# Optimization experiments

Hardware: AMD Instinct MI355X
Metric: run time of the kernel (lower is better)

Reference implementation:

```python
import jax, jax.numpy as jnp
import numpy as np

N_NODES = 50000


def gcn_conv(x, src, dst, W, b, n_nodes):
    # PyG GCNConv: add self-loops, symmetric normalization D^-1/2 (A+I) D^-1/2 (x W) + b
    E = src.shape[0]
    deg = jax.ops.segment_sum(jnp.ones((E,), x.dtype), dst, num_segments=n_nodes) + 1.0
    dinv = jax.lax.rsqrt(deg)
    h = x @ W  # [N, H]
    norm = dinv[src] * dinv[dst]  # [E]
    agg = jax.ops.segment_sum(h[src] * norm[:, None], dst, num_segments=n_nodes)
    agg = agg + h * (dinv * dinv)[:, None]  # self-loop contribution
    return agg + b


def setup_inputs() -> dict:
    key = jax.random.key(0)
    ks = jax.random.split(key, 16)
    N, E, D, H, T, O = N_NODES, 800000, 128, 128, 2, 1
    x = jax.random.normal(ks[0], (N, D), jnp.float32)
    edge_index = jax.random.randint(ks[1], (2, E), 0, N, jnp.int32)
    edge_attrs = jax.random.uniform(ks[2], (T, E, 7), jnp.float32)
    s = lambda k, sh: jax.random.normal(k, sh, jnp.float32) * (1.0 / np.sqrt(sh[0]))
    return {
        "x": x, "edge_index": edge_index, "edge_attrs": edge_attrs,
        "W1": s(ks[3], (D, H)), "b1": jnp.zeros((H,), jnp.float32),
        "W2": s(ks[4], (H, H)), "b2": jnp.zeros((H,), jnp.float32),
        "W3": s(ks[5], (H, H)), "b3": jnp.zeros((H,), jnp.float32),
        "We": s(ks[6], (2 * H + 7, H)), "be": jnp.zeros((H,), jnp.float32),
        "Wg": s(ks[7], (H, O)), "bg": jnp.zeros((O,), jnp.float32),
    }


def reference(x, edge_index, edge_attrs, W1, b1, W2, b2, W3, b3, We, be, Wg, bg):
    src, dst = edge_index[0], edge_index[1]
    n = x.shape[0]
    outputs = []
    for t in range(edge_attrs.shape[0]):  # small fixed T, x evolves across iterations
        edge_attr = edge_attrs[t]
        x = jax.nn.relu(gcn_conv(x, src, dst, W1, b1, n))
        x = jax.nn.relu(gcn_conv(x, src, dst, W2, b2, n))
        x = jax.nn.relu(gcn_conv(x, src, dst, W3, b3, n))
        # gather-concat-MLP-mean per edge
        edge_features = jnp.concatenate([x[src], x[dst], edge_attr], axis=1)
        edge_output = jax.nn.relu(edge_features @ We + be)
        graph_features = jnp.mean(edge_output, axis=0, keepdims=True)  # [1, H]
        outputs.append(graph_features @ Wg + bg)
        W1 = W2  # no-op placeholder removed below
        W1 = W1  # keep W1 unchanged
    return jnp.concatenate(outputs, axis=0)  # [T, output_dim]
```

## Files before the change

kernel.cpp:

```cpp
#include <hip/hip_runtime.h>
#include <hip/hip_bf16.h>


typedef __attribute__((ext_vector_type(8))) short bf16x8;
typedef __attribute__((ext_vector_type(4))) float f32x4;
typedef __attribute__((ext_vector_type(2))) float f32x2;

__device__ __forceinline__ unsigned short f2bf(float f) {
    union { float f; unsigned int u; } v; v.f = f;
    unsigned int r = v.u + 0x7fffu + ((v.u >> 16) & 1u);
    return (unsigned short)(r >> 16);
}
__device__ __forceinline__ unsigned int pk2bf(float lo, float hi) {
    return (unsigned int)f2bf(lo) | ((unsigned int)f2bf(hi) << 16);
}
__device__ __forceinline__ unsigned char f2fp8(float f) {
    return (unsigned char)(__builtin_amdgcn_cvt_pk_fp8_f32(f, f, 0, false) & 0xff);
}
__device__ __forceinline__ void fp8x4(unsigned int u, float* o) {
    f32x2 lo = __builtin_amdgcn_cvt_pk_f32_fp8(u, false);
    f32x2 hi = __builtin_amdgcn_cvt_pk_f32_fp8(u, true);
    o[0] = lo[0]; o[1] = lo[1]; o[2] = hi[0]; o[3] = hi[1];
}
__device__ __forceinline__ void de16add(uint4 v, float* a) {
    float t[4];
    fp8x4(v.x, t); a[0]+=t[0]; a[1]+=t[1]; a[2]+=t[2]; a[3]+=t[3];
    fp8x4(v.y, t); a[4]+=t[0]; a[5]+=t[1]; a[6]+=t[2]; a[7]+=t[3];
    fp8x4(v.z, t); a[8]+=t[0]; a[9]+=t[1]; a[10]+=t[2]; a[11]+=t[3];
    fp8x4(v.w, t); a[12]+=t[0]; a[13]+=t[1]; a[14]+=t[2]; a[15]+=t[3];
}

__global__ void to_bf16(const float* __restrict__ in, unsigned short* __restrict__ out, int n4)
{
    int i = blockIdx.x * 256 + threadIdx.x;
    if (i < n4) {
        float4 v = ((const float4*)in)[i];
        ushort4 o;
        o.x = f2bf(v.x); o.y = f2bf(v.y); o.z = f2bf(v.z); o.w = f2bf(v.w);
        ((ushort4*)out)[i] = o;
    }
}

__global__ void transpose_w(
    const float* __restrict__ W1, const float* __restrict__ W2,
    const float* __restrict__ W3, const float* __restrict__ We,
    unsigned short* __restrict__ T1, unsigned short* __restrict__ T2,
    unsigned short* __restrict__ T3, unsigned short* __restrict__ Tuv)
{
    const float* src; unsigned short* dst;
    switch (blockIdx.y) {
        case 0:  src = W1;             dst = T1;               break;
        case 1:  src = W2;             dst = T2;               break;
        case 2:  src = W3;             dst = T3;               break;
        case 3:  src = We;             dst = Tuv;              break;
        case 4:  src = We + 128 * 128; dst = Tuv + 128 * 128;  break;
        default: src = W2;             dst = Tuv + 256 * 128;  break;
    }
    for (int i = blockIdx.x * 256 + threadIdx.x; i < 128 * 128; i += 256 * gridDim.x) {
        int k = i >> 7, c = i & 127;
        dst[c * 128 + k] = f2bf(src[i]);
    }
}

__global__ __launch_bounds__(256) void mfma_matmul(
    const unsigned short* __restrict__ X, const unsigned short* __restrict__ Wt,
    unsigned char* __restrict__ out, const float* __restrict__ scale, int n_rows)
{
    const int wave = threadIdx.x >> 6;
    const int lane = threadIdx.x & 63;
    const int m = lane & 15;
    const int q = lane >> 4;
    const int r = blockIdx.x * 64 + wave * 16 + m;
    const bool rv = r < n_rows;

    f32x4 acc[8];
    #pragma unroll
    for (int i = 0; i < 8; ++i) acc[i] = (f32x4){0.f, 0.f, 0.f, 0.f};

    #pragma unroll
    for (int k0 = 0; k0 < 128; k0 += 32) {
        bf16x8 a = {};
        if (rv) a = *(const bf16x8*)(X + (size_t)r * 128 + k0 + q * 8);
        #pragma unroll
        for (int ct = 0; ct < 8; ++ct) {
            bf16x8 b = *(const bf16x8*)(Wt + (ct * 16 + m) * 128 + k0 + q * 8);
            acc[ct] = __builtin_amdgcn_mfma_f32_16x16x32_bf16(a, b, acc[ct], 0, 0, 0);
        }
    }

    #pragma unroll
    for (int reg = 0; reg < 4; ++reg) {
        int gr = blockIdx.x * 64 + wave * 16 + q * 4 + reg;
        if (gr >= n_rows) continue;
        float s = scale[gr];
        #pragma unroll
        for (int ct = 0; ct < 8; ++ct)
            out[(size_t)gr * 128 + ct * 16 + m] = f2fp8(acc[ct][reg] * s);
    }
}

#define FPAD 136
#define GN 32
#define ICAP 64
#define ISTR 72
__global__ __launch_bounds__(256) void fused_gm(
    const unsigned char* __restrict__ hs_in, const int* __restrict__ csr_src,
    const int* __restrict__ offs, const int* __restrict__ counts,
    const float* __restrict__ dinv, const float* __restrict__ bias,
    const unsigned short* __restrict__ Wt, int ncols, int uvcols,
    unsigned char* __restrict__ buv, unsigned char* __restrict__ bh, int n)
{
    __shared__ unsigned short xs[GN * FPAD];
    __shared__ int idxl[GN * ISTR];
    const int tid = threadIdx.x;
    const int row = tid >> 3;
    const int node = blockIdx.x * GN + row;
    const int lg = tid & 7;
    const int c16 = lg * 16;

    if (node < n) {
        const int off = offs[node];
        const int cnt = counts[node];
        const int cap = min(cnt, ICAP);

        for (int j = lg; j < cap; j += 8)
            idxl[row * ISTR + j] = csr_src[off + j];

        float a[16] = {};
        de16add(*(const uint4*)(hs_in + (size_t)node * 128 + c16), a);

        int j = 0;
        if (cap >= 4) {
            uint4 hA[4], hB[4];
            #pragma unroll
            for (int q = 0; q < 4; ++q)
                hA[q] = *(const uint4*)(hs_in + (size_t)idxl[row * ISTR + q] * 128 + c16);
            j = 4;
            for (; j + 4 <= cap; j += 4) {
                #pragma unroll
                for (int q = 0; q < 4; ++q)
                    hB[q] = *(const uint4*)(hs_in + (size_t)idxl[row * ISTR + j + q] * 128 + c16);
                #pragma unroll
                for (int q = 0; q < 4; ++q) de16add(hA[q], a);
                #pragma unroll
                for (int q = 0; q < 4; ++q) hA[q] = hB[q];
            }
            #pragma unroll
            for (int q = 0; q < 4; ++q) de16add(hA[q], a);
        }
        for (; j < cap; ++j)
            de16add(*(const uint4*)(hs_in + (size_t)idxl[row * ISTR + j] * 128 + c16), a);
        for (; j < cnt; ++j)
            de16add(*(const uint4*)(hs_in + (size_t)csr_src[off + j] * 128 + c16), a);

        float dn = dinv[node];
        #pragma unroll
        for (int i = 0; i < 4; ++i) {
            float4 bb = *(const float4*)(bias + c16 + i * 4);
            float r0 = fmaxf(fmaf(a[i*4+0], dn, bb.x), 0.f);
            float r1 = fmaxf(fmaf(a[i*4+1], dn, bb.y), 0.f);
            float r2 = fmaxf(fmaf(a[i*4+2], dn, bb.z), 0.f);
            float r3 = fmaxf(fmaf(a[i*4+3], dn, bb.w), 0.f);
            *(unsigned int*)&xs[row * FPAD + c16 + i*4 + 0] = pk2bf(r0, r1);
            *(unsigned int*)&xs[row * FPAD + c16 + i*4 + 2] = pk2bf(r2, r3);
        }
    }
    __syncthreads();

    const int wave = tid >> 6;
    const int lane = tid & 63;
    const int m = lane & 15;
    const int q = lane >> 4;
    const int rt = (wave & 1) * 16;
    const int nct = ncols >> 4;
    const int half = nct >> 1;
    const int ct0 = (wave >> 1) * half;

    for (int ci = 0; ci < half; ++ci) {
        const int ct = ct0 + ci;
        f32x4 acc = (f32x4){0.f, 0.f, 0.f, 0.f};
        #pragma unroll
        for (int k0 = 0; k0 < 128; k0 += 32) {
            bf16x8 a = *(const bf16x8*)&xs[(rt + m) * FPAD + k0 + q * 8];
            bf16x8 b = *(const bf16x8*)(Wt + (size_t)(ct * 16 + m) * 128 + k0 + q * 8);
            acc = __builtin_amdgcn_mfma_f32_16x16x32_bf16(a, b, acc, 0, 0, 0);
        }
        const int col = ct * 16 + m;
        #pragma unroll
        for (int reg = 0; reg < 4; ++reg) {
            int nd = blockIdx.x * GN + rt + q * 4 + reg;
            if (nd >= n) continue;
            if (col < uvcols)
                buv[(size_t)nd * 256 + col] = f2fp8(acc[reg]);
            else
                bh[(size_t)nd * 128 + col - uvcols] = f2fp8(acc[reg] * dinv[nd]);
        }
    }
}

#define EM_CHUNK 256
__global__ __launch_bounds__(256) void edge_mlp(
    const unsigned char* __restrict__ uv, const int* __restrict__ src,
    const int* __restrict__ dst, const float* __restrict__ ea,
    const float* __restrict__ We_e, const float* __restrict__ be,
    const float* __restrict__ Wg, float* __restrict__ acc, int E)
{
    const int tid  = threadIdx.x;
    const int lane = tid & 31;
    const int g    = tid >> 5;
    const int c4   = lane * 4;

    __shared__ float eas[EM_CHUNK * 7];
    __shared__ int   ss[EM_CHUNK];
    __shared__ int   ds[EM_CHUNK];
    __shared__ float red[256];

    float4 w[7];
    #pragma unroll
    for (int i = 0; i < 7; ++i)
        w[i] = *(const float4*)(We_e + i * 128 + c4);
    const float4 be4 = *(const float4*)(be + c4);
    const float4 wg4 = *(const float4*)(Wg + c4);

    float4 part = make_float4(0.f, 0.f, 0.f, 0.f);

    for (int base = blockIdx.x * EM_CHUNK; base < E; base += gridDim.x * EM_CHUNK) {
        const int nch = min(EM_CHUNK, E - base);
        for (int i = tid; i < nch * 7; i += 256)
            eas[i] = ea[(size_t)base * 7 + i];
        for (int i = tid; i < nch; i += 256) {
            ss[i] = src[base + i];
            ds[i] = dst[base + i];
        }
        __syncthreads();

        auto ev = [&](int j) {
            unsigned int us = *(const unsigned int*)(uv + (size_t)ss[j] * 256 + c4);
            unsigned int vs = *(const unsigned int*)(uv + (size_t)ds[j] * 256 + 128 + c4);
            float uf[4], vf[4];
            fp8x4(us, uf); fp8x4(vs, vf);
            const float* eav = &eas[j * 7];
            float4 val;
            val.x = uf[0] + vf[0] + be4.x;
            val.y = uf[1] + vf[1] + be4.y;
            val.z = uf[2] + vf[2] + be4.z;
            val.w = uf[3] + vf[3] + be4.w;
            #pragma unroll
            for (int i = 0; i < 7; ++i) {
                float e = eav[i];
                val.x = fmaf(e, w[i].x, val.x);
                val.y = fmaf(e, w[i].y, val.y);
                val.z = fmaf(e, w[i].z, val.z);
                val.w = fmaf(e, w[i].w, val.w);
            }
            part.x += fmaxf(val.x, 0.f);
            part.y += fmaxf(val.y, 0.f);
            part.z += fmaxf(val.z, 0.f);
            part.w += fmaxf(val.w, 0.f);
        };

        int j = g;
        for (; j + 32 <= nch; j += 32) {
            ev(j); ev(j + 8); ev(j + 16); ev(j + 24);
        }
        for (; j < nch; j += 8)
            ev(j);
        __syncthreads();
    }

    float p = part.x * wg4.x + part.y * wg4.y + part.z * wg4.z + part.w * wg4.w;
    red[tid] = p;
    __syncthreads();
    for (int s = 128; s > 0; s >>= 1) {
        if (tid < s) red[tid] += red[tid + s];
        __syncthreads();
    }
    if (tid == 0) atomicAdd(acc, red[0]);
}

__global__ void count_edges(const int* __restrict__ dst, int* __restrict__ counts, int E)
{
    int e = blockIdx.x * 256 + threadIdx.x;
    if (e < E) atomicAdd(&counts[dst[e]], 1);
}

__global__ void compute_dinv(const int* __restrict__ counts, float* __restrict__ dinv, int n)
{
    int i = blockIdx.x * 256 + threadIdx.x;
    if (i < n) dinv[i] = rsqrtf((float)counts[i] + 1.0f);
}

__global__ void scan1(const int* __restrict__ counts, int* __restrict__ scanned,
                      int* __restrict__ btot, int n)
{
    __shared__ int sh[256];
    int i = blockIdx.x * 256 + threadIdx.x;
    int v = (i < n) ? counts[i] : 0;
    sh[threadIdx.x] = v;
    __syncthreads();
    for (int off = 1; off < 256; off <<= 1) {
        int t = (threadIdx.x >= off) ? sh[threadIdx.x - off] : 0;
        __syncthreads();
        sh[threadIdx.x] += t;
        __syncthreads();
    }
    if (i < n) scanned[i] = sh[threadIdx.x] - v;
    if (threadIdx.x == 255) btot[blockIdx.x] = sh[255];
}

__global__ void scan2(int* __restrict__ btot, int nb)
{
    __shared__ int sh[256];
    int v = (threadIdx.x < nb) ? btot[threadIdx.x] : 0;
    sh[threadIdx.x] = v;
    __syncthreads();
    for (int off = 1; off < 256; off <<= 1) {
        int t = (threadIdx.x >= off) ? sh[threadIdx.x - off] : 0;
        __syncthreads();
        sh[threadIdx.x] += t;
        __syncthreads();
    }
    if (threadIdx.x < nb) btot[threadIdx.x] = sh[threadIdx.x] - v;
}

__global__ void scan3(const int* __restrict__ scanned, const int* __restrict__ btot,
                      int* __restrict__ offs, int* __restrict__ cursor, int n)
{
    int i = blockIdx.x * 256 + threadIdx.x;
    if (i < n) {
        int o = scanned[i] + btot[blockIdx.x];
        offs[i] = o;
        cursor[i] = o;
    }
}

__global__ void fill_csr(const int* __restrict__ src, const int* __restrict__ dst,
                         int* __restrict__ cursor, int* __restrict__ csr_src, int E)
{
    int e = blockIdx.x * 256 + threadIdx.x;
    if (e < E) {
        int slot = atomicAdd(&cursor[dst[e]], 1);
        csr_src[slot] = src[e];
    }
}

__global__ void write_out(const float* __restrict__ acc, const float* __restrict__ bg,
                          float* __restrict__ out, float invE, int T)
{
    int t = threadIdx.x;
    if (t < T) out[t] = acc[t] * invE + bg[0];
}


extern "C" void kernel_launch(void* const* d_in, const int* in_sizes, int n_in,
                              void* d_out, int out_size, void* d_ws, size_t ws_size,
                              hipStream_t stream)
{
    const float* x   = (const float*)d_in[0];
    const int*  eidx = (const int*)d_in[1];
    const float* ea  = (const float*)d_in[2];
    const float* W1  = (const float*)d_in[3];
    const float* b1  = (const float*)d_in[4];
    const float* W2  = (const float*)d_in[5];
    const float* b2  = (const float*)d_in[6];
    const float* W3  = (const float*)d_in[7];
    const float* b3  = (const float*)d_in[8];
    const float* We  = (const float*)d_in[9];
    const float* be  = (const float*)d_in[10];
    const float* Wg  = (const float*)d_in[11];
    const float* bg  = (const float*)d_in[12];

    const int N = in_sizes[0] / 128;
    const int E = in_sizes[1] / 2;
    const int T = in_sizes[2] / (E * 7);
    const int* src = eidx;
    const int* dst = eidx + E;

    char* wsp = (char*)d_ws;
    auto alloc = [&](size_t bytes) -> char* {
        char* p = wsp;
        wsp += (bytes + 255) / 256 * 256;
        return p;
    };
    int*   counts  = (int*)alloc((size_t)N * 4);
    int*   offs    = (int*)alloc((size_t)N * 4);
    int*   cursor  = (int*)alloc((size_t)N * 4);
    int*   scanned = (int*)alloc((size_t)N * 4);
    int*   btot    = (int*)alloc(1024);
    int*   csr_src = (int*)alloc((size_t)E * 4);
    float* dinv    = (float*)alloc((size_t)N * 4);
    float* acc     = (float*)alloc(256);
    unsigned short* X0  = (unsigned short*)alloc((size_t)N * 128 * 2);
    unsigned char*  Bh0 = (unsigned char*)alloc((size_t)N * 128);
    unsigned char*  Bh1 = (unsigned char*)alloc((size_t)N * 128);
    unsigned char*  Buv = (unsigned char*)alloc((size_t)N * 256);
    unsigned short* T1  = (unsigned short*)alloc(128 * 128 * 2);
    unsigned short* T2  = (unsigned short*)alloc(128 * 128 * 2);
    unsigned short* T3  = (unsigned short*)alloc(128 * 128 * 2);
    unsigned short* Tuv = (unsigned short*)alloc(384 * 128 * 2);

    hipMemsetAsync(counts, 0, (size_t)N * 4, stream);
    hipMemsetAsync(acc, 0, (size_t)T * 4, stream);

    to_bf16<<<(N * 128 / 4 + 255) / 256, 256, 0, stream>>>(x, X0, N * 128 / 4);
    transpose_w<<<dim3(8, 6), 256, 0, stream>>>(W1, W2, W3, We, T1, T2, T3, Tuv);

    count_edges<<<(E + 255) / 256, 256, 0, stream>>>(dst, counts, E);
    compute_dinv<<<(N + 255) / 256, 256, 0, stream>>>(counts, dinv, N);
    const int nb = (N + 255) / 256;
    scan1<<<nb, 256, 0, stream>>>(counts, scanned, btot, N);
    scan2<<<1, 256, 0, stream>>>(btot, nb);
    scan3<<<nb, 256, 0, stream>>>(scanned, btot, offs, cursor, N);
    fill_csr<<<(E + 255) / 256, 256, 0, stream>>>(src, dst, cursor, csr_src, E);

    const int mmb = (N + 63) / 64;
    const int fgb = (N + GN - 1) / GN;
    const int emb = (E + EM_CHUNK - 1) / EM_CHUNK;

    unsigned char* hcur = Bh0;
    unsigned char* hnxt = Bh1;

    for (int t = 0; t < T; ++t) {
        if (t == 0) {
            mfma_matmul<<<mmb, 256, 0, stream>>>(X0, T1, hcur, dinv, N);
        }
        fused_gm<<<fgb, 256, 0, stream>>>(hcur, csr_src, offs, counts, dinv, b1,
                                          T2, 128, 0, Buv, hnxt, N);
        { unsigned char* tmp = hcur; hcur = hnxt; hnxt = tmp; }
        fused_gm<<<fgb, 256, 0, stream>>>(hcur, csr_src, offs, counts, dinv, b2,
                                          T3, 128, 0, Buv, hnxt, N);
        { unsigned char* tmp = hcur; hcur = hnxt; hnxt = tmp; }
        bool last = (t == T - 1);
        fused_gm<<<fgb, 256, 0, stream>>>(hcur, csr_src, offs, counts, dinv, b3,
                                          Tuv, last ? 256 : 384, 256, Buv, hnxt, N);
        if (!last) { unsigned char* tmp = hcur; hcur = hnxt; hnxt = tmp; }

        edge_mlp<<<emb, 256, 0, stream>>>(Buv, src, dst, ea + (size_t)t * E * 7,
                                          We + 256 * 128, be, Wg, acc + t, E);
    }
    write_out<<<1, 64, 0, stream>>>(acc, bg, (float*)d_out, 1.0f / (float)E, T);
}
```

Measured before the change: 599.0 us.

## Balance gather-aggregation across threads by splitting block edges evenly with LDS atomics

Replaces per-node edge loops in the fused gather+matmul kernel with an edge-balanced scheme. All edges of the block's 32 nodes are staged in shared memory, split evenly across the 32 thread groups, and accumulated into a shared fp32 buffer via atomic adds at each node boundary. This targets load imbalance from skewed degrees within a block. The cost is LDS atomics, zeroing the accumulator, an extra barrier and slow overflow handling beyond the edge cap.

After: 861.9 us. 1.44x slower.

```diff
diff --git a/kernel.cpp b/kernel.cpp
--- a/kernel.cpp
+++ b/kernel.cpp
@@ -101,8 +101,8 @@
 
 #define FPAD 136
 #define GN 32
-#define ICAP 64
-#define ISTR 72
+#define ACCP 129
+#define ECAP 1536
 __global__ __launch_bounds__(256) void fused_gm(
     const unsigned char* __restrict__ hs_in, const int* __restrict__ csr_src,
     const int* __restrict__ offs, const int* __restrict__ counts,
@@ -110,59 +110,121 @@
     const unsigned short* __restrict__ Wt, int ncols, int uvcols,
     unsigned char* __restrict__ buv, unsigned char* __restrict__ bh, int n)
 {
-    __shared__ unsigned short xs[GN * FPAD];
-    __shared__ int idxl[GN * ISTR];
+    __shared__ float accs[GN * ACCP];
+    __shared__ __align__(16) unsigned char ubuf[GN * FPAD * 2];
+    int* idxs = (int*)ubuf;
+    unsigned char* dls = ubuf + ECAP * 4;
+    int* offs_s = (int*)(ubuf + ECAP * 5);
+    unsigned short* xs = (unsigned short*)ubuf;
+
     const int tid = threadIdx.x;
-    const int row = tid >> 3;
-    const int node = blockIdx.x * GN + row;
-    const int lg = tid & 7;
+    const int G   = tid >> 3;
+    const int lg  = tid & 7;
     const int c16 = lg * 16;
-
-    if (node < n) {
-        const int off = offs[node];
-        const int cnt = counts[node];
-        const int cap = min(cnt, ICAP);
-
-        for (int j = lg; j < cap; j += 8)
-            idxl[row * ISTR + j] = csr_src[off + j];
-
-        float a[16] = {};
-        de16add(*(const uint4*)(hs_in + (size_t)node * 128 + c16), a);
-
-        int j = 0;
-        if (cap >= 4) {
+    const int node0 = blockIdx.x * GN;
+    const int nn = min(GN, n - node0);
+
+    const int e_last = node0 + nn - 1;
+    const int e0 = offs[node0];
+    const int e1 = offs[e_last] + counts[e_last];
+    const int ne = e1 - e0;
+    const int ns = min(ne, ECAP);
+
+    for (int i = tid; i < ns; i += 256) idxs[i] = csr_src[e0 + i];
+
+    uint4 sv = {};
+    if (G < nn) {
+        const int off = offs[node0 + G];
+        const int cnt = counts[node0 + G];
+        if (lg == 0) offs_s[G] = off;
+        const int base = off - e0;
+        for (int j = lg; j < cnt && base + j < ECAP; j += 8)
+            dls[base + j] = (unsigned char)G;
+        sv = *(const uint4*)(hs_in + (size_t)(node0 + G) * 128 + c16);
+    }
+    if (tid == 0) offs_s[nn] = e1;
+    for (int i = tid; i < GN * ACCP; i += 256) accs[i] = 0.f;
+    __syncthreads();
+
+    const int js = (ns * G) >> 5;
+    const int je = (ns * (G + 1)) >> 5;
+
+    float a[16] = {};
+    int cur = 0;
+    auto flush = [&](int d) {
+        #pragma unroll
+        for (int i = 0; i < 16; ++i) {
+            atomicAdd(&accs[d * ACCP + c16 + i], a[i]);
+            a[i] = 0.f;
+        }
+    };
+
+    int j = js;
+    if (je - js > 0) {
+        cur = dls[js];
+        if (je - js >= 4) {
             uint4 hA[4], hB[4];
+            int dA[4], dB[4];
             #pragma unroll
-            for (int q = 0; q < 4; ++q)
-                hA[q] = *(const uint4*)(hs_in + (size_t)idxl[row * ISTR + q] * 128 + c16);
-            j = 4;
-            for (; j + 4 <= cap; j += 4) {
+            for (int q = 0; q < 4; ++q) {
+                dA[q] = dls[js + q];
+                hA[q] = *(const uint4*)(hs_in + (size_t)idxs[js + q] * 128 + c16);
+            }
+            j = js + 4;
+            for (; j + 4 <= je; j += 4) {
                 #pragma unroll
-                for (int q = 0; q < 4; ++q)
-                    hB[q] = *(const uint4*)(hs_in + (size_t)idxl[row * ISTR + j + q] * 128 + c16);
+                for (int q = 0; q < 4; ++q) {
+                    dB[q] = dls[j + q];
+                    hB[q] = *(const uint4*)(hs_in + (size_t)idxs[j + q] * 128 + c16);
+                }
                 #pragma unroll
-                for (int q = 0; q < 4; ++q) de16add(hA[q], a);
+                for (int q = 0; q < 4; ++q) {
+                    if (dA[q] != cur) { flush(cur); cur = dA[q]; }
+                    de16add(hA[q], a);
+                }
                 #pragma unroll
-                for (int q = 0; q < 4; ++q) hA[q] = hB[q];
+                for (int q = 0; q < 4; ++q) { hA[q] = hB[q]; dA[q] = dB[q]; }
             }
             #pragma unroll
-            for (int q = 0; q < 4; ++q) de16add(hA[q], a);
-        }
-        for (; j < cap; ++j)
-            de16add(*(const uint4*)(hs_in + (size_t)idxl[row * ISTR + j] * 128 + c16), a);
-        for (; j < cnt; ++j)
-            de16add(*(const uint4*)(hs_in + (size_t)csr_src[off + j] * 128 + c16), a);
-
-        float dn = dinv[node];
+            for (int q = 0; q < 4; ++q) {
+                if (dA[q] != cur) { flush(cur); cur = dA[q]; }
+                de16add(hA[q], a);
+            }
+        }
+        for (; j < je; ++j) {
+            int d = dls[j];
+            if (d != cur) { flush(cur); cur = d; }
+            de16add(*(const uint4*)(hs_in + (size_t)idxs[j] * 128 + c16), a);
+        }
+        flush(cur);
+    }
+    for (int j2 = ns + G; j2 < ne; j2 += GN) {
+        const int gidx = csr_src[e0 + j2];
+        const int ge = e0 + j2;
+        int d = 0;
+        while (d + 1 < nn && offs_s[d + 1] <= ge) ++d;
+        de16add(*(const uint4*)(hs_in + (size_t)gidx * 128 + c16), a);
+        flush(d);
+    }
+    __syncthreads();
+
+    if (G < nn) {
+        float s16[16] = {};
+        de16add(sv, s16);
+        const float dn = dinv[node0 + G];
         #pragma unroll
         for (int i = 0; i < 4; ++i) {
             float4 bb = *(const float4*)(bias + c16 + i * 4);
-            float r0 = fmaxf(fmaf(a[i*4+0], dn, bb.x), 0.f);
-            float r1 = fmaxf(fmaf(a[i*4+1], dn, bb.y), 0.f);
-            float r2 = fmaxf(fmaf(a[i*4+2], dn, bb.z), 0.f);
-            float r3 = fmaxf(fmaf(a[i*4+3], dn, bb.w), 0.f);
-            *(unsigned int*)&xs[row * FPAD + c16 + i*4 + 0] = pk2bf(r0, r1);
-            *(unsigned int*)&xs[row * FPAD + c16 + i*4 + 2] = pk2bf(r2, r3);
+            float v0 = accs[G * ACCP + c16 + i * 4 + 0] + s16[i * 4 + 0];
+            float v1 = accs[G * ACCP + c16 + i * 4 + 1] + s16[i * 4 + 1];
+            float v2 = accs[G * ACCP + c16 + i * 4 + 2] + s16[i * 4 + 2];
+            float v3 = accs[G * ACCP + c16 + i * 4 + 3] + s16[i * 4 + 3];
+            float r0 = fmaxf(fmaf(v0, dn, bb.x), 0.f);
+            float r1 = fmaxf(fmaf(v1, dn, bb.y), 0.f);
+            float r2 = fmaxf(fmaf(v2, dn, bb.z), 0.f);
+            float r3 = fmaxf(fmaf(v3, dn, bb.w), 0.f);
+            *(unsigned int*)&xs[G * FPAD + c16 + i * 4 + 0] = pk2bf(r0, r1);
+            *(unsigned int*)&xs[G * FPAD + c16 + i * 4 + 2] = pk2bf(r2, r3);
         }
     }
     __syncthreads();
@@ -181,9 +243,9 @@
         f32x4 acc = (f32x4){0.f, 0.f, 0.f, 0.f};
         #pragma unroll
         for (int k0 = 0; k0 < 128; k0 += 32) {
-            bf16x8 a = *(const bf16x8*)&xs[(rt + m) * FPAD + k0 + q * 8];
+            bf16x8 av = *(const bf16x8*)&xs[(rt + m) * FPAD + k0 + q * 8];
             bf16x8 b = *(const bf16x8*)(Wt + (size_t)(ct * 16 + m) * 128 + k0 + q * 8);
-            acc = __builtin_amdgcn_mfma_f32_16x16x32_bf16(a, b, acc, 0, 0, 0);
+            acc = __builtin_amdgcn_mfma_f32_16x16x32_bf16(av, b, acc, 0, 0, 0);
         }
         const int col = ct * 16 + m;
         #pragma unroll
```

## Use 16 nodes per block with 16 threads per node in fused gather-matmul

Applied to the files above, without the earlier changes.

The fused gather-and-transform kernel now handles 16 nodes per block instead of 32. Each node is split across 16 lanes that each load 8 fp8 bytes, where before 8 lanes each loaded 16 bytes. Launch bounds now request 8 blocks per CU, and the MFMA stage gives each wave one 16-row tile and a quarter of the column tiles. The goal is more parallelism in the latency-bound neighbor gather, with fewer registers per thread and better occupancy. In exchange, each gather is narrower and every block reloads the weight tiles, so the grid has twice as many blocks and weight traffic doubles.

Result: faster. 558.5 us (-6.8%).

```diff
diff --git a/kernel.cpp b/kernel.cpp
--- a/kernel.cpp
+++ b/kernel.cpp
@@ -22,12 +22,10 @@
     f32x2 hi = __builtin_amdgcn_cvt_pk_f32_fp8(u, true);
     o[0] = lo[0]; o[1] = lo[1]; o[2] = hi[0]; o[3] = hi[1];
 }
-__device__ __forceinline__ void de16add(uint4 v, float* a) {
+__device__ __forceinline__ void de8add(uint2 v, float* a) {
     float t[4];
     fp8x4(v.x, t); a[0]+=t[0]; a[1]+=t[1]; a[2]+=t[2]; a[3]+=t[3];
     fp8x4(v.y, t); a[4]+=t[0]; a[5]+=t[1]; a[6]+=t[2]; a[7]+=t[3];
-    fp8x4(v.z, t); a[8]+=t[0]; a[9]+=t[1]; a[10]+=t[2]; a[11]+=t[3];
-    fp8x4(v.w, t); a[12]+=t[0]; a[13]+=t[1]; a[14]+=t[2]; a[15]+=t[3];
 }
 
 __global__ void to_bf16(const float* __restrict__ in, unsigned short* __restrict__ out, int n4)
@@ -100,10 +98,10 @@
 }
 
 #define FPAD 136
-#define GN 32
+#define GN 16
 #define ICAP 64
 #define ISTR 72
-__global__ __launch_bounds__(256) void fused_gm(
+__global__ __launch_bounds__(256, 8) void fused_gm(
     const unsigned char* __restrict__ hs_in, const int* __restrict__ csr_src,
     const int* __restrict__ offs, const int* __restrict__ counts,
     const float* __restrict__ dinv, const float* __restrict__ bias,
@@ -113,57 +111,64 @@
     __shared__ unsigned short xs[GN * FPAD];
     __shared__ int idxl[GN * ISTR];
     const int tid = threadIdx.x;
-    const int row = tid >> 3;
+    const int row = tid >> 4;
     const int node = blockIdx.x * GN + row;
-    const int lg = tid & 7;
-    const int c16 = lg * 16;
+    const int lg = tid & 15;
+    const int c8 = lg * 8;
 
     if (node < n) {
         const int off = offs[node];
         const int cnt = counts[node];
         const int cap = min(cnt, ICAP);
 
-        for (int j = lg; j < cap; j += 8)
+        for (int j = lg; j < cap; j += 16)
             idxl[row * ISTR + j] = csr_src[off + j];
 
-        float a[16] = {};
-        de16add(*(const uint4*)(hs_in + (size_t)node * 128 + c16), a);
-
+        const uint2 sv = *(const uint2*)(hs_in + (size_t)node * 128 + c8);
+
+        float a[8] = {};
         int j = 0;
         if (cap >= 4) {
-            uint4 hA[4], hB[4];
+            uint2 hA[4], hB[4];
             #pragma unroll
             for (int q = 0; q < 4; ++q)
-                hA[q] = *(const uint4*)(hs_in + (size_t)idxl[row * ISTR + q] * 128 + c16);
+                hA[q] = *(const uint2*)(hs_in + (size_t)idxl[row * ISTR + q] * 128 + c8);
+            de8add(sv, a);
             j = 4;
             for (; j + 4 <= cap; j += 4) {
                 #pragma unroll
                 for (int q = 0; q < 4; ++q)
-                    hB[q] = *(const uint4*)(hs_in + (size_t)idxl[row * ISTR + j + q] * 128 + c16);
+                    hB[q] = *(const uint2*)(hs_in + (size_t)idxl[row * ISTR + j + q] * 128 + c8);
                 #pragma unroll
-                for (int q = 0; q < 4; ++q) de16add(hA[q], a);
+                for (int q = 0; q < 4; ++q) de8add(hA[q], a);
                 #pragma unroll
                 for (int q = 0; q < 4; ++q) hA[q] = hB[q];
             }
             #pragma unroll
-            for (int q = 0; q < 4; ++q) de16add(hA[q], a);
+            for (int q = 0; q < 4; ++q) de8add(hA[q], a);
+        } else {
+            de8add(sv, a);
         }
         for (; j < cap; ++j)
-            de16add(*(const uint4*)(hs_in + (size_t)idxl[row * ISTR + j] * 128 + c16), a);
+            de8add(*(const uint2*)(hs_in + (size_t)idxl[row * ISTR + j] * 128 + c8), a);
         for (; j < cnt; ++j)
-            de16add(*(const uint4*)(hs_in + (size_t)csr_src[off + j] * 128 + c16), a);
-
-        float dn = dinv[node];
-        #pragma unroll
-        for (int i = 0; i < 4; ++i) {
-            float4 bb = *(const float4*)(bias + c16 + i * 4);
-            float r0 = fmaxf(fmaf(a[i*4+0], dn, bb.x), 0.f);
-            float r1 = fmaxf(fmaf(a[i*4+1], dn, bb.y), 0.f);
-            float r2 = fmaxf(fmaf(a[i*4+2], dn, bb.z), 0.f);
-            float r3 = fmaxf(fmaf(a[i*4+3], dn, bb.w), 0.f);
-            *(unsigned int*)&xs[row * FPAD + c16 + i*4 + 0] = pk2bf(r0, r1);
-            *(unsigned int*)&xs[row * FPAD + c16 + i*4 + 2] = pk2bf(r2, r3);
-        }
+            de8add(*(const uint2*)(hs_in + (size_t)csr_src[off + j] * 128 + c8), a);
+
+        const float dn = dinv[node];
+        const float4 b0 = *(const float4*)(bias + c8);
+        const float4 b1v = *(const float4*)(bias + c8 + 4);
+        float r0 = fmaxf(fmaf(a[0], dn, b0.x), 0.f);
+        float r1 = fmaxf(fmaf(a[1], dn, b0.y), 0.f);
+        float r2 = fmaxf(fmaf(a[2], dn, b0.z), 0.f);
+        float r3 = fmaxf(fmaf(a[3], dn, b0.w), 0.f);
+        float r4 = fmaxf(fmaf(a[4], dn, b1v.x), 0.f);
+        float r5 = fmaxf(fmaf(a[5], dn, b1v.y), 0.f);
+        float r6 = fmaxf(fmaf(a[6], dn, b1v.z), 0.f);
+        float r7 = fmaxf(fmaf(a[7], dn, b1v.w), 0.f);
+        uint4 w;
+        w.x = pk2bf(r0, r1); w.y = pk2bf(r2, r3);
+        w.z = pk2bf(r4, r5); w.w = pk2bf(r6, r7);
+        *(uint4*)&xs[row * FPAD + c8] = w;
     }
     __syncthreads();
 
@@ -171,24 +176,23 @@
     const int lane = tid & 63;
     const int m = lane & 15;
     const int q = lane >> 4;
-    const int rt = (wave & 1) * 16;
     const int nct = ncols >> 4;
-    const int half = nct >> 1;
-    const int ct0 = (wave >> 1) * half;
-
-    for (int ci = 0; ci < half; ++ci) {
+    const int per = nct >> 2;
+    const int ct0 = wave * per;
+
+    for (int ci = 0; ci < per; ++ci) {
         const int ct = ct0 + ci;
         f32x4 acc = (f32x4){0.f, 0.f, 0.f, 0.f};
         #pragma unroll
         for (int k0 = 0; k0 < 128; k0 += 32) {
-            bf16x8 a = *(const bf16x8*)&xs[(rt + m) * FPAD + k0 + q * 8];
+            bf16x8 a = *(const bf16x8*)&xs[m * FPAD + k0 + q * 8];
             bf16x8 b = *(const bf16x8*)(Wt + (size_t)(ct * 16 + m) * 128 + k0 + q * 8);
             acc = __builtin_amdgcn_mfma_f32_16x16x32_bf16(a, b, acc, 0, 0, 0);
         }
         const int col = ct * 16 + m;
         #pragma unroll
         for (int reg = 0; reg < 4; ++reg) {
-            int nd = blockIdx.x * GN + rt + q * 4 + reg;
+            int nd = blockIdx.x * GN + q * 4 + reg;
             if (nd >= n) continue;
             if (col < uvcols)
                 buv[(size_t)nd * 256 + col] = f2fp8(acc[reg]);
```
